# Performance work log

Hardware: AMD Instinct MI355X
Metric: run time of the kernel (lower is better)

## Reference

```python
import jax, jax.numpy as jnp
import numpy as np

N_HEADS = 16
HEAD_SIZE = 64
N_EMBD = N_HEADS * HEAD_SIZE  # 1024
B, T = 4, 2048


def setup_inputs() -> dict:
    key = jax.random.key(0)
    kx, kq, kk, kv, kp = jax.random.split(key, 5)
    s = 1.0 / np.sqrt(N_EMBD)
    return {
        "x": jax.random.normal(kx, (B, T, N_EMBD), dtype=jnp.float32),
        "Wq": jax.random.normal(kq, (N_EMBD, N_HEADS * HEAD_SIZE), dtype=jnp.float32) * s,
        "Wk": jax.random.normal(kk, (N_EMBD, N_HEADS * HEAD_SIZE), dtype=jnp.float32) * s,
        "Wv": jax.random.normal(kv, (N_EMBD, N_HEADS * HEAD_SIZE), dtype=jnp.float32) * s,
        "Wp": jax.random.normal(kp, (N_HEADS * HEAD_SIZE, N_EMBD), dtype=jnp.float32) * s,
    }


def reference(x, Wq, Wk, Wv, Wp):
    Bb, Tt, C = x.shape
    H, hs = N_HEADS, HEAD_SIZE
    # QKV projections (no bias), split heads: (B, H, T, hs)
    q = (x @ Wq).reshape(Bb, Tt, H, hs).transpose(0, 2, 1, 3)
    k = (x @ Wk).reshape(Bb, Tt, H, hs).transpose(0, 2, 1, 3)
    v = (x @ Wv).reshape(Bb, Tt, H, hs).transpose(0, 2, 1, 3)
    scores = jnp.einsum("bhqd,bhkd->bhqk", q, k) / np.sqrt(hs).astype(np.float32)
    causal = jnp.tril(jnp.ones((Tt, Tt), dtype=bool))
    scores = jnp.where(causal, scores, -jnp.inf)
    attn = jax.nn.softmax(scores, axis=-1)  # dropout p=0 -> identity
    o = jnp.einsum("bhqk,bhkd->bhqd", attn, v)  # (B, H, T, hs)
    # Faithfully replicate torch's view/transpose/view sequence:
    o = o.reshape(Bb, Tt, H * hs)          # raw reshape of (B,H,T,hs) buffer
    o = jnp.swapaxes(o, 1, 2)               # (B, H*hs, T)
    o = o.reshape(Bb, Tt, H * hs)           # contiguous().view
    return o @ Wp
```

## Files before the change

### kernel.cpp

```cpp
#include <hip/hip_runtime.h>

typedef unsigned short ush;
typedef unsigned int u32;
typedef __attribute__((ext_vector_type(4))) float f32x4;
typedef __attribute__((ext_vector_type(8))) short short8;
typedef __attribute__((ext_vector_type(8))) ush ushx8;
typedef __attribute__((ext_vector_type(4))) ush ushx4;

#define GAS __attribute__((address_space(1)))
#define LAS __attribute__((address_space(3)))

__device__ __forceinline__ void gl_lds16(const void* g, void* l) {
  __builtin_amdgcn_global_load_lds((const GAS void*)g, (LAS void*)l, 16, 0, 0);
}

__device__ __forceinline__ ush f2bf(float f) {
  union { float f; unsigned int u; } x; x.f = f;
  unsigned int r = x.u + 0x7fffu + ((x.u >> 16) & 1u);
  return (ush)(r >> 16);
}
__device__ __forceinline__ u32 fbits(float f) {
  union { float f; u32 u; } x; x.f = f; return x.u;
}

#define NEG_BIG (-1.0e4f)
#define SCL 0.18033688f

__device__ __forceinline__ int kkey(int row) { return ((row & 3) + (row >> 2)) & 3; }

__global__ __launch_bounds__(256) void k_prep(
    const float* __restrict__ X, const float* __restrict__ W0,
    const float* __restrict__ W1, const float* __restrict__ W2,
    const float* __restrict__ W3, ush* __restrict__ Xb, ush* __restrict__ Wt) {
  __shared__ ush Ts[64][72];
  const int bx = blockIdx.x;
  if (bx < 4096) {
    int idx = bx * 256 + threadIdx.x;
    int base = idx * 8;
    f32x4 a = *(const f32x4*)(X + base);
    f32x4 b = *(const f32x4*)(X + base + 4);
    ushx8 o;
#pragma unroll
    for (int q = 0; q < 4; ++q) { o[q] = f2bf(a[q]); o[4 + q] = f2bf(b[q]); }
    *(ushx8*)(Xb + base) = o;
    return;
  }
  const int bid = bx - 4096;
  const int z = bid >> 8;
  const int k0 = (bid & 15) * 64, n0 = ((bid >> 4) & 15) * 64;
  const float* W = (z == 0) ? W0 : (z == 1) ? W1 : (z == 2) ? W2 : W3;
  ush* Ot = Wt + (size_t)z * 1048576;
  const int rr = threadIdx.x >> 4, cc = threadIdx.x & 15;
#pragma unroll
  for (int i = 0; i < 4; ++i) {
    int row = i * 16 + rr;
    f32x4 v = *(const f32x4*)(W + (size_t)(k0 + row) * 1024 + n0 + cc * 4);
#pragma unroll
    for (int q = 0; q < 4; ++q) Ts[row][cc * 4 + q] = f2bf(v[q]);
  }
  __syncthreads();
#pragma unroll
  for (int i = 0; i < 4; ++i) {
    int n = i * 16 + rr;
    ushx4 o;
#pragma unroll
    for (int q = 0; q < 4; ++q) o[q] = Ts[cc * 4 + q][n];
    *(ushx4*)(Ot + (size_t)(n0 + n) * 1024 + k0 + cc * 4) = o;
  }
}

__global__ __launch_bounds__(512, 2) void k_gemm_qkv(
    const ush* __restrict__ X, const ush* __restrict__ Wt,
    ush* __restrict__ QKV, ush* __restrict__ Vtg) {
  __shared__ __align__(16) ush sm[36864];
  const int tid = threadIdx.x;
  const int w = tid >> 6, l = tid & 63, lr = l & 15, lg = l >> 4;
  const int wm = w >> 2, wn = w & 3;
  const int mt = blockIdx.x, nt = blockIdx.y;
  const int which = nt >> 3, n0 = (nt & 7) * 128;
  const ush* Ag = X + (size_t)mt * 256 * 1024;
  const ush* Bg = Wt + (size_t)which * 1048576 + (size_t)n0 * 1024;
  int aoff[2], boff;
  {
#pragma unroll
    for (int it = 0; it < 2; ++it) {
      int ch = it * 512 + tid, row = ch >> 2, g = ch & 3;
      aoff[it] = row * 1024 + ((g ^ kkey(row)) << 3);
    }
    int row = tid >> 2, g = tid & 3;
    boff = row * 1024 + ((g ^ kkey(row)) << 3);
  }
  f32x4 acc[8][2] = {};

  auto issueS = [&](int kt, int st) {
    const ush* Asrc = Ag + kt * 32;
    const ush* Bsrc = Bg + kt * 32;
    ush* base = sm + st * 12288;
#pragma unroll
    for (int it = 0; it < 2; ++it)
      gl_lds16(Asrc + aoff[it], base + ((size_t)it * 512 + tid) * 8);
    gl_lds16(Bsrc + boff, base + 8192 + (size_t)tid * 8);
  };

  issueS(0, 0);
  issueS(1, 1);
  int st = 0, st2 = 2;
  for (int t = 0; t < 32; ++t) {
    if (t < 31) {
      asm volatile("s_waitcnt vmcnt(3)" ::: "memory");
    } else {
      asm volatile("s_waitcnt vmcnt(0)" ::: "memory");
    }
    __syncthreads();
    if (t + 2 < 32) issueS(t + 2, st2);
    const ush* Ab = sm + st * 12288;
    const ush* Bb = sm + st * 12288 + 8192;
    short8 fb[2];
#pragma unroll
    for (int ni = 0; ni < 2; ++ni) {
      int row = wn * 32 + ni * 16 + lr;
      fb[ni] = *(const short8*)(Bb + row * 32 + ((lg ^ kkey(row)) << 3));
    }
#pragma unroll
    for (int qm = 0; qm < 4; ++qm) {
      short8 fa[2];
#pragma unroll
      for (int m2 = 0; m2 < 2; ++m2) {
        int row = wm * 128 + (qm * 2 + m2) * 16 + lr;
        fa[m2] = *(const short8*)(Ab + row * 32 + ((lg ^ kkey(row)) << 3));
      }
      __builtin_amdgcn_s_setprio(1);
#pragma unroll
      for (int m2 = 0; m2 < 2; ++m2)
#pragma unroll
        for (int ni = 0; ni < 2; ++ni)
          acc[qm * 2 + m2][ni] = __builtin_amdgcn_mfma_f32_16x16x32_bf16(
              fa[m2], fb[ni], acc[qm * 2 + m2][ni], 0, 0, 0);
      __builtin_amdgcn_s_setprio(0);
    }
    st = (st == 2) ? 0 : st + 1;
    st2 = (st2 == 2) ? 0 : st2 + 1;
  }
  __syncthreads();
  ush* Ct = sm;
#pragma unroll
  for (int mi = 0; mi < 8; ++mi)
#pragma unroll
    for (int ni = 0; ni < 2; ++ni)
#pragma unroll
      for (int j = 0; j < 4; ++j)
        Ct[(wm * 128 + mi * 16 + lg * 4 + j) * 128 + wn * 32 + ni * 16 + lr] =
            f2bf(acc[mi][ni][j]);
  __syncthreads();
  const int m0 = mt * 256, b = m0 >> 11, t0 = m0 & 2047, h0 = n0 >> 6;
  if (which == 2) {
    const int cc = tid & 127, rq = tid >> 7;
    const int hsel = cc >> 6, d = cc & 63;
    ush* dst = Vtg + (size_t)(b * 16 + h0 + hsel) * 131072 + (size_t)d * 2048 +
               t0 + rq * 64;
#pragma unroll
    for (int ch = 0; ch < 8; ++ch) {
      ushx8 v;
#pragma unroll
      for (int k = 0; k < 8; ++k) v[k] = Ct[(rq * 64 + ch * 8 + k) * 128 + cc];
      *(ushx8*)(dst + ch * 8) = v;
    }
  } else {
    ush* Om = QKV + (size_t)which * 8388608;
#pragma unroll
    for (int it = 0; it < 8; ++it) {
      int c = it * 512 + tid;
      int hsel = c >> 11;
      int cc = c & 2047;
      int r = cc >> 3;
      int c8 = (cc & 7) * 8;
      ushx8 v = *(const ushx8*)(Ct + r * 128 + hsel * 64 + c8);
      *(ushx8*)(Om + ((size_t)(b * 16 + h0 + hsel) * 2048 + t0 + r) * 64 + c8) = v;
    }
  }
}

__global__ __launch_bounds__(256) void k_attn(
    const ush* __restrict__ Q, const ush* __restrict__ K,
    const ush* __restrict__ Vg, ush* __restrict__ O) {
  __shared__ __align__(16) ush Ks[2][4096];
  __shared__ __align__(16) ush Vs[2][4096];
  __shared__ __align__(16) ush Pl[8][1024];
  const int lid = blockIdx.x + 16 * blockIdx.y;
  const int qta = (lid >> 3) & 15;
  const int bh  = ((lid >> 7) << 3) | (lid & 7);
  const int qtb = 31 - qta;
  const size_t hb = (size_t)bh * (2048 * 64);
  const ush* Qh = Q + hb;
  const ush* Kh = K + hb;
  const ush* Vh = Vg + hb;
  const int tid = threadIdx.x, w = tid >> 6, l = tid & 63, lr = l & 15, lg = l >> 4;
  const int q0a = qta * 64 + w * 16, q0b = qtb * 64 + w * 16;

  short8 qfa[2], qfb[2];
#pragma unroll
  for (int s = 0; s < 2; ++s) {
    qfa[s] = *(const short8*)(Qh + (size_t)(q0a + lr) * 64 + s * 32 + lg * 8);
    qfb[s] = *(const short8*)(Qh + (size_t)(q0b + lr) * 64 + s * 32 + lg * 8);
  }
  f32x4 acca[4] = {}, accb[4] = {};
  float la[4] = {0.f, 0.f, 0.f, 0.f}, lb[4] = {0.f, 0.f, 0.f, 0.f};

  int koff[2], voff[2];
#pragma unroll
  for (int it = 0; it < 2; ++it) {
    int ch = it * 256 + tid;
    int r = ch >> 3, g = ch & 7;
    koff[it] = r * 64 + ((g ^ (r & 7)) << 3);
    int keyv = ((r & 7) + (r >> 3)) & 7;
    voff[it] = r * 2048 + ((g ^ keyv) << 3);
  }
  auto issueStage = [&](int c, int buf) {
#pragma unroll
    for (int it = 0; it < 2; ++it) {
      int ch = it * 256 + tid;
      gl_lds16(Kh + (size_t)c * 4096 + koff[it], &Ks[buf][ch * 8]);
      gl_lds16(Vh + c * 64 + voff[it], &Vs[buf][ch * 8]);
    }
  };

  auto ctile = [&](const ush* Kc, const ush* Vc, const short8* qf,
                   f32x4* acc, float* lrow, bool diag, ush* PlW) {
    f32x4 sf[4] = {};
#pragma unroll
    for (int s = 0; s < 2; ++s)
#pragma unroll
      for (int f = 0; f < 4; ++f) {
        int kv = f * 16 + lr;
        short8 kf = *(const short8*)(Kc + kv * 64 + (((s * 4 + lg) ^ (kv & 7)) << 3));
        sf[f] = __builtin_amdgcn_mfma_f32_16x16x32_bf16(qf[s], kf, sf[f], 0, 0, 0);
      }
#pragma unroll
    for (int f = 0; f < 4; ++f)
#pragma unroll
      for (int j = 0; j < 4; ++j) {
        float vv = sf[f][j] * SCL;
        if (diag && (f * 16 + lr) > (w * 16 + lg * 4 + j)) vv = NEG_BIG;
        sf[f][j] = __builtin_amdgcn_exp2f(vv);
      }
#pragma unroll
    for (int j = 0; j < 4; ++j)
      lrow[j] += (sf[0][j] + sf[1][j]) + (sf[2][j] + sf[3][j]);
#pragma unroll
    for (int f = 0; f < 4; ++f)
#pragma unroll
      for (int j = 0; j < 4; ++j) {
        int q = lg * 4 + j;
        PlW[q * 64 + ((f * 16 + lr) ^ ((q & 7) << 3))] = (ush)(fbits(sf[f][j]) >> 16);
      }
#pragma unroll
    for (int s = 0; s < 2; ++s) {
      short8 pf = *(const short8*)(PlW + lr * 64 + (((s * 4 + lg) ^ (lr & 7)) << 3));
#pragma unroll
      for (int db = 0; db < 4; ++db) {
        int dv = db * 16 + lr;
        int keyv = ((dv & 7) + (dv >> 3)) & 7;
        short8 vf = *(const short8*)(Vc + dv * 64 + (((s * 4 + lg) ^ keyv) << 3));
        acc[db] = __builtin_amdgcn_mfma_f32_16x16x32_bf16(pf, vf, acc[db], 0, 0, 0);
      }
    }
  };

  issueStage(0, 0);
  int cur = 0;
  for (int c = 0; c <= qtb; ++c) {
    asm volatile("s_waitcnt vmcnt(0)" ::: "memory");
    __syncthreads();
    if (c < qtb) issueStage(c + 1, cur ^ 1);
    const ush* Kc = Ks[cur];
    const ush* Vc = Vs[cur];
    if (c <= qta) ctile(Kc, Vc, qfa, acca, la, c == qta, Pl[w]);
    ctile(Kc, Vc, qfb, accb, lb, c == qtb, Pl[4 + w]);
    cur ^= 1;
  }

#pragma unroll
  for (int msk = 1; msk <= 8; msk <<= 1)
#pragma unroll
    for (int j = 0; j < 4; ++j) {
      la[j] += __shfl_xor(la[j], msk);
      lb[j] += __shfl_xor(lb[j], msk);
    }
  float ia[4], ib[4];
#pragma unroll
  for (int j = 0; j < 4; ++j) {
    ia[j] = __builtin_amdgcn_rcpf(la[j]);
    ib[j] = __builtin_amdgcn_rcpf(lb[j]);
  }
  ush* Oh = O + hb;
#pragma unroll
  for (int db = 0; db < 4; ++db)
#pragma unroll
    for (int j = 0; j < 4; ++j) {
      Oh[(size_t)(q0a + lg * 4 + j) * 64 + db * 16 + lr] = f2bf(acca[db][j] * ia[j]);
      Oh[(size_t)(q0b + lg * 4 + j) * 64 + db * 16 + lr] = f2bf(accb[db][j] * ib[j]);
    }
}

__global__ __launch_bounds__(256) void k_gather(const ush* __restrict__ Ob, ush* __restrict__ Mb) {
  __shared__ ush Ls[2][128][68];
  const int jh = blockIdx.x, tau = blockIdx.y, b = blockIdx.z;
  const int tid = threadIdx.x;
#pragma unroll
  for (int it = 0; it < 8; ++it) {
    int c = it * 256 + tid;
    int r = c >> 3, d8 = (c & 7) * 8;
    int esel = r >> 7, jlow = r & 127;
    ushx8 v = *(const ushx8*)(Ob +
        ((size_t)(b * 16 + jh + esel * 8) * 2048 + jlow * 16 + tau) * 64 + d8);
    *(ushx8*)(&Ls[esel][jlow][d8]) = v;
  }
  __syncthreads();
  const int wv = tid >> 6, l = tid & 63;
  const int e = wv >> 1, jhalf = wv & 1, d = l;
  ush* Mrow = Mb + (size_t)b * 2097152 +
              (size_t)(128 * tau + 2 * d + e) * 1024 + jh * 128 + jhalf * 64;
#pragma unroll
  for (int ch = 0; ch < 8; ++ch) {
    ushx8 v;
#pragma unroll
    for (int k = 0; k < 8; ++k) v[k] = Ls[e][jhalf * 64 + ch * 8 + k][d];
    *(ushx8*)(Mrow + ch * 8) = v;
  }
}

__global__ __launch_bounds__(512, 2) void k_gemm_out(
    const ush* __restrict__ A, const ush* __restrict__ Bt, float* __restrict__ Out) {
  __shared__ __align__(16) ush sm[36864];
  const int tid = threadIdx.x;
  const int w = tid >> 6, l = tid & 63, lr = l & 15, lg = l >> 4;
  const int wm = w >> 2, wn = w & 3;
  const int mt = blockIdx.x, nt = blockIdx.y;
  const int n0 = nt * 128;
  const ush* Ag = A + (size_t)mt * 256 * 1024;
  const ush* Bg = Bt + (size_t)n0 * 1024;
  int aoff[2], boff;
  {
#pragma unroll
    for (int it = 0; it < 2; ++it) {
      int ch = it * 512 + tid, row = ch >> 2, g = ch & 3;
      aoff[it] = row * 1024 + ((g ^ kkey(row)) << 3);
    }
    int row = tid >> 2, g = tid & 3;
    boff = row * 1024 + ((g ^ kkey(row)) << 3);
  }
  f32x4 acc[8][2] = {};

  auto issueS = [&](int kt, int st) {
    const ush* Asrc = Ag + kt * 32;
    const ush* Bsrc = Bg + kt * 32;
    ush* base = sm + st * 12288;
#pragma unroll
    for (int it = 0; it < 2; ++it)
      gl_lds16(Asrc + aoff[it], base + ((size_t)it * 512 + tid) * 8);
    gl_lds16(Bsrc + boff, base + 8192 + (size_t)tid * 8);
  };

  issueS(0, 0);
  issueS(1, 1);
  int st = 0, st2 = 2;
  for (int t = 0; t < 32; ++t) {
    if (t < 31) {
      asm volatile("s_waitcnt vmcnt(3)" ::: "memory");
    } else {
      asm volatile("s_waitcnt vmcnt(0)" ::: "memory");
    }
    __syncthreads();
    if (t + 2 < 32) issueS(t + 2, st2);
    const ush* Ab = sm + st * 12288;
    const ush* Bb = sm + st * 12288 + 8192;
    short8 fb[2];
#pragma unroll
    for (int ni = 0; ni < 2; ++ni) {
      int row = wn * 32 + ni * 16 + lr;
      fb[ni] = *(const short8*)(Bb + row * 32 + ((lg ^ kkey(row)) << 3));
    }
#pragma unroll
    for (int qm = 0; qm < 4; ++qm) {
      short8 fa[2];
#pragma unroll
      for (int m2 = 0; m2 < 2; ++m2) {
        int row = wm * 128 + (qm * 2 + m2) * 16 + lr;
        fa[m2] = *(const short8*)(Ab + row * 32 + ((lg ^ kkey(row)) << 3));
      }
      __builtin_amdgcn_s_setprio(1);
#pragma unroll
      for (int m2 = 0; m2 < 2; ++m2)
#pragma unroll
        for (int ni = 0; ni < 2; ++ni)
          acc[qm * 2 + m2][ni] = __builtin_amdgcn_mfma_f32_16x16x32_bf16(
              fa[m2], fb[ni], acc[qm * 2 + m2][ni], 0, 0, 0);
      __builtin_amdgcn_s_setprio(0);
    }
    st = (st == 2) ? 0 : st + 1;
    st2 = (st2 == 2) ? 0 : st2 + 1;
  }
  const int m0 = mt * 256;
#pragma unroll
  for (int mi = 0; mi < 8; ++mi)
#pragma unroll
    for (int ni = 0; ni < 2; ++ni)
#pragma unroll
      for (int j = 0; j < 4; ++j)
        Out[(size_t)(m0 + wm * 128 + mi * 16 + lg * 4 + j) * 1024 +
            n0 + wn * 32 + ni * 16 + lr] = acc[mi][ni][j];
}

extern "C" void kernel_launch(void* const* d_in, const int* in_sizes, int n_in,
                              void* d_out, int out_size, void* d_ws, size_t ws_size,
                              hipStream_t stream) {
  const float* x  = (const float*)d_in[0];
  const float* wq = (const float*)d_in[1];
  const float* wk = (const float*)d_in[2];
  const float* wv = (const float*)d_in[3];
  const float* wp = (const float*)d_in[4];
  float* out = (float*)d_out;
  char* ws = (char*)d_ws;
  ush* xb  = (ush*)ws;
  ush* wt  = (ush*)(ws + 16777216);
  ush* qkv = (ush*)(ws + 25165824);
  ush* vtg = (ush*)(ws + 75497472);
  ush* ob  = qkv;
  ush* mb  = xb;

  k_prep<<<dim3(5120), 256, 0, stream>>>(x, wq, wk, wv, wp, xb, wt);
  k_gemm_qkv<<<dim3(32, 24), 512, 0, stream>>>(xb, wt, qkv, vtg);
  k_attn<<<dim3(16, 64), 256, 0, stream>>>(qkv, qkv + 8388608, vtg, ob);
  k_gather<<<dim3(8, 16, 4), 256, 0, stream>>>(ob, mb);
  k_gemm_out<<<dim3(32, 8), 512, 0, stream>>>(mb, wt + 3145728, out);
}
```

Baseline: 195.3 us.

## Load K fragments directly to registers, fold softmax scale into Q projection

K tiles are no longer staged through LDS with global_load_lds. Each wave now reads its K MFMA fragments straight from global memory into registers every iteration, and only V stays double-buffered in LDS. The softmax scale is applied to Q in the projection GEMM epilogue, which removes a multiply per score, and MFMA sections are wrapped in s_setprio. The risks are that the K loads are issued after the wait and consumed right away, so their latency is exposed, and that each wave re-reads the whole K tile from L2.

```diff
diff --git a/kernel.cpp b/kernel.cpp
--- a/kernel.cpp
+++ b/kernel.cpp
@@ -142,6 +142,7 @@
     st2 = (st2 == 2) ? 0 : st2 + 1;
   }
   __syncthreads();
+  const float oscale = (which == 0) ? SCL : 1.0f;
   ush* Ct = sm;
 #pragma unroll
   for (int mi = 0; mi < 8; ++mi)
@@ -150,7 +151,7 @@
 #pragma unroll
       for (int j = 0; j < 4; ++j)
         Ct[(wm * 128 + mi * 16 + lg * 4 + j) * 128 + wn * 32 + ni * 16 + lr] =
-            f2bf(acc[mi][ni][j]);
+            f2bf(acc[mi][ni][j] * oscale);
   __syncthreads();
   const int m0 = mt * 256, b = m0 >> 11, t0 = m0 & 2047, h0 = n0 >> 6;
   if (which == 2) {
@@ -183,7 +184,6 @@
 __global__ __launch_bounds__(256) void k_attn(
     const ush* __restrict__ Q, const ush* __restrict__ K,
     const ush* __restrict__ Vg, ush* __restrict__ O) {
-  __shared__ __align__(16) ush Ks[2][4096];
   __shared__ __align__(16) ush Vs[2][4096];
   __shared__ __align__(16) ush Pl[8][1024];
   const int lid = blockIdx.x + 16 * blockIdx.y;
@@ -206,40 +206,47 @@
   f32x4 acca[4] = {}, accb[4] = {};
   float la[4] = {0.f, 0.f, 0.f, 0.f}, lb[4] = {0.f, 0.f, 0.f, 0.f};
 
-  int koff[2], voff[2];
+  int voff[2];
 #pragma unroll
   for (int it = 0; it < 2; ++it) {
     int ch = it * 256 + tid;
     int r = ch >> 3, g = ch & 7;
-    koff[it] = r * 64 + ((g ^ (r & 7)) << 3);
     int keyv = ((r & 7) + (r >> 3)) & 7;
     voff[it] = r * 2048 + ((g ^ keyv) << 3);
   }
-  auto issueStage = [&](int c, int buf) {
+  auto issueV = [&](int c, int buf) {
 #pragma unroll
     for (int it = 0; it < 2; ++it) {
       int ch = it * 256 + tid;
-      gl_lds16(Kh + (size_t)c * 4096 + koff[it], &Ks[buf][ch * 8]);
       gl_lds16(Vh + c * 64 + voff[it], &Vs[buf][ch * 8]);
     }
   };
 
-  auto ctile = [&](const ush* Kc, const ush* Vc, const short8* qf,
+  short8 kf[2][4];
+  auto loadKf = [&](int c) {
+#pragma unroll
+    for (int s = 0; s < 2; ++s)
+#pragma unroll
+      for (int f = 0; f < 4; ++f)
+        kf[s][f] = *(const short8*)(Kh + ((size_t)c * 64 + f * 16 + lr) * 64 +
+                                    s * 32 + lg * 8);
+  };
+
+  auto ctile = [&](const ush* Vc, const short8* qf,
                    f32x4* acc, float* lrow, bool diag, ush* PlW) {
     f32x4 sf[4] = {};
+    __builtin_amdgcn_s_setprio(1);
 #pragma unroll
     for (int s = 0; s < 2; ++s)
 #pragma unroll
-      for (int f = 0; f < 4; ++f) {
-        int kv = f * 16 + lr;
-        short8 kf = *(const short8*)(Kc + kv * 64 + (((s * 4 + lg) ^ (kv & 7)) << 3));
-        sf[f] = __builtin_amdgcn_mfma_f32_16x16x32_bf16(qf[s], kf, sf[f], 0, 0, 0);
-      }
+      for (int f = 0; f < 4; ++f)
+        sf[f] = __builtin_amdgcn_mfma_f32_16x16x32_bf16(qf[s], kf[s][f], sf[f], 0, 0, 0);
+    __builtin_amdgcn_s_setprio(0);
 #pragma unroll
     for (int f = 0; f < 4; ++f)
 #pragma unroll
       for (int j = 0; j < 4; ++j) {
-        float vv = sf[f][j] * SCL;
+        float vv = sf[f][j];
         if (diag && (f * 16 + lr) > (w * 16 + lg * 4 + j)) vv = NEG_BIG;
         sf[f][j] = __builtin_amdgcn_exp2f(vv);
       }
@@ -253,6 +260,7 @@
         int q = lg * 4 + j;
         PlW[q * 64 + ((f * 16 + lr) ^ ((q & 7) << 3))] = (ush)(fbits(sf[f][j]) >> 16);
       }
+    __builtin_amdgcn_s_setprio(1);
 #pragma unroll
     for (int s = 0; s < 2; ++s) {
       short8 pf = *(const short8*)(PlW + lr * 64 + (((s * 4 + lg) ^ (lr & 7)) << 3));
@@ -264,18 +272,19 @@
         acc[db] = __builtin_amdgcn_mfma_f32_16x16x32_bf16(pf, vf, acc[db], 0, 0, 0);
       }
     }
+    __builtin_amdgcn_s_setprio(0);
   };
 
-  issueStage(0, 0);
+  issueV(0, 0);
   int cur = 0;
   for (int c = 0; c <= qtb; ++c) {
     asm volatile("s_waitcnt vmcnt(0)" ::: "memory");
     __syncthreads();
-    if (c < qtb) issueStage(c + 1, cur ^ 1);
-    const ush* Kc = Ks[cur];
+    if (c < qtb) issueV(c + 1, cur ^ 1);
+    loadKf(c);
     const ush* Vc = Vs[cur];
-    if (c <= qta) ctile(Kc, Vc, qfa, acca, la, c == qta, Pl[w]);
-    ctile(Kc, Vc, qfb, accb, lb, c == qtb, Pl[4 + w]);
+    if (c <= qta) ctile(Vc, qfa, acca, la, c == qta, Pl[w]);
+    ctile(Vc, qfb, accb, lb, c == qtb, Pl[4 + w]);
     cur ^= 1;
   }
 
```

Measured after the change: 242.2 us. 1.24x slower.
